# Kernel optimization log

Measured on AMD Instinct MI355X. Metric: run time of the kernel, lower is better.

The kernel has to match this reference:

```python
import jax, jax.numpy as jnp
import numpy as np

K = 3
STRIDE = 1
PAD = 1
C_IN = 128
C_OUT = 256

def setup_inputs() -> dict:
    key = jax.random.key(0)
    kx, kw, kb = jax.random.split(key, 3)
    x = jax.random.normal(kx, (32, C_IN, 56, 56), dtype=jnp.float32)
    # torch init: uniform(-1/K, 1/K) for kernels, uniform(-1/sqrt(Cout), 1/sqrt(Cout)) for bias
    kernels = jax.random.uniform(kw, (C_OUT, C_IN, K, K), dtype=jnp.float32,
                                 minval=-1.0 / K, maxval=1.0 / K)
    b = jax.random.uniform(kb, (C_OUT,), dtype=jnp.float32,
                           minval=-1.0 / C_OUT ** 0.5, maxval=1.0 / C_OUT ** 0.5)
    return {"x": x, "kernels": kernels, "b": b}

def reference(x, kernels, b):
    # Same math as the im2col broadcast-matmul + channel-sum: a standard 2D conv
    # with zero padding, expressed as one contracted GEMM via conv_general_dilated.
    out = jax.lax.conv_general_dilated(
        x, kernels,
        window_strides=(STRIDE, STRIDE),
        padding=((PAD, PAD), (PAD, PAD)),
        dimension_numbers=("NCHW", "OIHW", "NCHW"),
    )
    return out + b.reshape(1, C_OUT, 1, 1)
```

## Files before the change

kernel.cpp:

```cpp
#include <hip/hip_runtime.h>
#include <hip/hip_bf16.h>

#define NB   32
#define CIN  128
#define COUT 256
#define HH   56
#define WW   56

typedef __attribute__((ext_vector_type(8))) short short8;
typedef __attribute__((ext_vector_type(4))) float f32x4;

__device__ __forceinline__ unsigned short f2bf(float f) {
    unsigned int u = __builtin_bit_cast(unsigned int, f);
    u = u + 0x7fffu + ((u >> 16) & 1u);
    return (unsigned short)(u >> 16);
}

__global__ __launch_bounds__(256) void wpose_kernel(const float* __restrict__ w,
                                                    unsigned short* __restrict__ wt2) {
    int q = blockIdx.x * 256 + threadIdx.x;
    if (q >= 36 * 16 * 64 * 8) return;
    int j = q & 7;
    int l = (q >> 3) & 63;
    int f = (q >> 9) & 15;
    int s = q >> 13;
    int g = l >> 4, r = l & 15;
    int t = s >> 2, cc = s & 3;
    int o = f * 16 + r;
    int c = cc * 32 + g * 8 + j;
    wt2[q] = f2bf(w[((size_t)o * CIN + c) * 9 + t]);
}

__global__ __launch_bounds__(1024, 4) void conv_mfma_kernel(
        const float* __restrict__ x,
        const unsigned short* __restrict__ wt2,
        const float* __restrict__ bias,
        float* __restrict__ out) {
    __shared__ unsigned short ldsB[6 * 16 * 58 * 8];

    const int tid  = threadIdx.x;
    const int h0   = blockIdx.x * 4, n = blockIdx.y;
    const int wid  = tid >> 6, lane = tid & 63;
    const int wm   = wid >> 1, wn = wid & 1;
    const int g    = lane >> 4, r = lane & 15;

    for (int i = tid; i < 6 * 16 * 58; i += 1024) {
        uint4 z = {0u, 0u, 0u, 0u};
        *(uint4*)&ldsB[(size_t)i * 8] = z;
    }
    __syncthreads();

    {
        const float* xn = x + (size_t)n * CIN * HH * WW;
        for (int i = tid; i < 6 * 64 * 14; i += 1024) {
            int w4  = i % 14;
            int t1  = i / 14;
            int cp  = t1 & 63;
            int row = t1 >> 6;
            int hs  = h0 + row - 1;
            if ((unsigned)hs < HH) {
                const float* src = xn + ((size_t)(2 * cp) * HH + hs) * WW + 4 * w4;
                float4 va = *(const float4*)src;
                float4 vb = *(const float4*)(src + HH * WW);
                int gc = cp >> 2, e = cp & 3;
                #pragma unroll
                for (int j = 0; j < 4; ++j) {
                    int wpos = 4 * w4 + j + 1;
                    unsigned int pk = (unsigned int)f2bf(((const float*)&va)[j])
                                    | ((unsigned int)f2bf(((const float*)&vb)[j]) << 16);
                    ((unsigned int*)ldsB)[((row * 16 + gc) * 58 + wpos) * 4 + e] = pk;
                }
            }
        }
    }
    __syncthreads();

    int lo[7];
    #pragma unroll
    for (int ni = 0; ni < 7; ++ni) {
        int c  = ni * 16 + r;
        int hr = (c >= 56) ? 1 : 0;
        lo[ni] = hr * (16 * 58) + (c - hr * 56);
    }

    f32x4 acc[2][7];
    #pragma unroll
    for (int mi = 0; mi < 2; ++mi)
        #pragma unroll
        for (int ni = 0; ni < 7; ++ni)
            #pragma unroll
            for (int v = 0; v < 4; ++v) acc[mi][ni][v] = 0.f;

    const short8* abase = (const short8*)wt2 + (size_t)(wm * 2) * 64 + lane;

    #pragma unroll
    for (int t = 0; t < 9; ++t) {
        const int kh = t / 3, kw = t % 3;
        #pragma unroll
        for (int cc = 0; cc < 4; ++cc) {
            const int s  = t * 4 + cc;
            const int gc = cc * 4 + g;
            const int bb = (((wn * 2 + kh) * 16 + gc) * 58 + kw);

            short8 a[2];
            #pragma unroll
            for (int mi = 0; mi < 2; ++mi)
                a[mi] = abase[(size_t)s * 1024 + mi * 64];

            short8 b[7];
            #pragma unroll
            for (int ni = 0; ni < 7; ++ni)
                b[ni] = *(const short8*)&ldsB[(size_t)(bb + lo[ni]) * 8];

            #pragma unroll
            for (int mi = 0; mi < 2; ++mi)
                #pragma unroll
                for (int ni = 0; ni < 7; ++ni)
                    acc[mi][ni] = __builtin_amdgcn_mfma_f32_16x16x32_bf16(
                        a[mi], b[ni], acc[mi][ni], 0, 0, 0);
        }
    }

    #pragma unroll
    for (int mi = 0; mi < 2; ++mi) {
        const int o0 = wm * 32 + mi * 16 + 4 * g;
        const float4 bv = *(const float4*)&bias[o0];
        #pragma unroll
        for (int ni = 0; ni < 7; ++ni) {
            const int c  = ni * 16 + r;
            const int hr = (c >= 56) ? 1 : 0;
            const int h  = h0 + wn * 2 + hr;
            const int w  = c - hr * 56;
            #pragma unroll
            for (int v = 0; v < 4; ++v) {
                out[((size_t)(n * COUT + o0 + v) * HH + h) * WW + w] =
                    acc[mi][ni][v] + ((const float*)&bv)[v];
            }
        }
    }
}

extern "C" void kernel_launch(void* const* d_in, const int* in_sizes, int n_in,
                              void* d_out, int out_size, void* d_ws, size_t ws_size,
                              hipStream_t stream) {
    const float* x  = (const float*)d_in[0];
    const float* wk = (const float*)d_in[1];
    const float* b  = (const float*)d_in[2];
    float* out = (float*)d_out;

    unsigned short* wt2 = (unsigned short*)d_ws;

    wpose_kernel<<<(36 * 16 * 64 * 8 + 255) / 256, 256, 0, stream>>>(wk, wt2);
    dim3 gc(14, NB);
    conv_mfma_kernel<<<gc, 1024, 0, stream>>>(x, wt2, b, out);
    (void)ws_size; (void)in_sizes; (void)n_in; (void)out_size;
}
```

Baseline: 77.41 us.

## Re-tile conv waves to 128 output channels by 32 pixels and simplify staging

Changes the per-wave tile from 32 output channels by 112 pixels to 128 channels by 32 pixels, spread over 2x8 waves. Each wave now loads 8 A fragments from global weights and only 2 B fragments from LDS per step, cutting LDS reads but raising global weight traffic per wave. The last wave column pads to 256 pixels and masks stores, so some MFMA work is wasted. Input staging switches from float4 loads to scalar per-element loads with one lane per channel pair, which may lower global load efficiency.

```diff
diff --git a/kernel.cpp b/kernel.cpp
--- a/kernel.cpp
+++ b/kernel.cpp
@@ -41,7 +41,7 @@
     const int tid  = threadIdx.x;
     const int h0   = blockIdx.x * 4, n = blockIdx.y;
     const int wid  = tid >> 6, lane = tid & 63;
-    const int wm   = wid >> 1, wn = wid & 1;
+    const int wm   = wid >> 3, wn = wid & 7;
     const int g    = lane >> 4, r = lane & 15;
 
     for (int i = tid; i < 6 * 16 * 58; i += 1024) {
@@ -52,89 +52,85 @@
 
     {
         const float* xn = x + (size_t)n * CIN * HH * WW;
-        for (int i = tid; i < 6 * 64 * 14; i += 1024) {
-            int w4  = i % 14;
-            int t1  = i / 14;
-            int cp  = t1 & 63;
-            int row = t1 >> 6;
+        const int cp = tid & 63, e = cp & 3, gcq = cp >> 2;
+        const float* pc = xn + (size_t)(2 * cp) * (HH * WW);
+        for (int rw = tid >> 6; rw < 6 * 56; rw += 16) {
+            int row = rw / 56, w = rw - row * 56;
             int hs  = h0 + row - 1;
             if ((unsigned)hs < HH) {
-                const float* src = xn + ((size_t)(2 * cp) * HH + hs) * WW + 4 * w4;
-                float4 va = *(const float4*)src;
-                float4 vb = *(const float4*)(src + HH * WW);
-                int gc = cp >> 2, e = cp & 3;
-                #pragma unroll
-                for (int j = 0; j < 4; ++j) {
-                    int wpos = 4 * w4 + j + 1;
-                    unsigned int pk = (unsigned int)f2bf(((const float*)&va)[j])
-                                    | ((unsigned int)f2bf(((const float*)&vb)[j]) << 16);
-                    ((unsigned int*)ldsB)[((row * 16 + gc) * 58 + wpos) * 4 + e] = pk;
-                }
+                const float* p = pc + hs * WW + w;
+                unsigned int pk = (unsigned int)f2bf(p[0])
+                                | ((unsigned int)f2bf(p[HH * WW]) << 16);
+                ((unsigned int*)ldsB)[((row * 16 + gcq) * 58 + (w + 1)) * 4 + e] = pk;
             }
         }
     }
     __syncthreads();
 
-    int lo[7];
+    int hrv[2], wv[2], base2[2];
+    bool ok[2];
     #pragma unroll
-    for (int ni = 0; ni < 7; ++ni) {
-        int c  = ni * 16 + r;
-        int hr = (c >= 56) ? 1 : 0;
-        lo[ni] = hr * (16 * 58) + (c - hr * 56);
+    for (int ni = 0; ni < 2; ++ni) {
+        int c = wn * 32 + ni * 16 + r;
+        ok[ni] = (c < 224);
+        int hr, w;
+        if (ok[ni]) { hr = c / 56; w = c - hr * 56; }
+        else        { hr = 3;      w = c & 31; }
+        hrv[ni] = hr; wv[ni] = w;
+        base2[ni] = hr * 928 + g * 58 + w;
     }
 
-    f32x4 acc[2][7];
+    f32x4 acc[8][2];
     #pragma unroll
-    for (int mi = 0; mi < 2; ++mi)
+    for (int mi = 0; mi < 8; ++mi)
         #pragma unroll
-        for (int ni = 0; ni < 7; ++ni)
+        for (int ni = 0; ni < 2; ++ni)
             #pragma unroll
             for (int v = 0; v < 4; ++v) acc[mi][ni][v] = 0.f;
 
-    const short8* abase = (const short8*)wt2 + (size_t)(wm * 2) * 64 + lane;
+    const short8* abase = (const short8*)wt2 + (size_t)(wm * 8) * 64 + lane;
 
     #pragma unroll
     for (int t = 0; t < 9; ++t) {
         const int kh = t / 3, kw = t % 3;
         #pragma unroll
         for (int cc = 0; cc < 4; ++cc) {
-            const int s  = t * 4 + cc;
-            const int gc = cc * 4 + g;
-            const int bb = (((wn * 2 + kh) * 16 + gc) * 58 + kw);
+            const int s = t * 4 + cc;
 
-            short8 a[2];
+            short8 a[8];
             #pragma unroll
-            for (int mi = 0; mi < 2; ++mi)
+            for (int mi = 0; mi < 8; ++mi)
                 a[mi] = abase[(size_t)s * 1024 + mi * 64];
 
-            short8 b[7];
+            const int koff = kh * 928 + cc * 232 + kw;
+            short8 b[2];
             #pragma unroll
-            for (int ni = 0; ni < 7; ++ni)
-                b[ni] = *(const short8*)&ldsB[(size_t)(bb + lo[ni]) * 8];
+            for (int ni = 0; ni < 2; ++ni)
+                b[ni] = *(const short8*)&ldsB[(size_t)(base2[ni] + koff) * 8];
 
             #pragma unroll
-            for (int mi = 0; mi < 2; ++mi)
+            for (int mi = 0; mi < 8; ++mi)
                 #pragma unroll
-                for (int ni = 0; ni < 7; ++ni)
+                for (int ni = 0; ni < 2; ++ni)
                     acc[mi][ni] = __builtin_amdgcn_mfma_f32_16x16x32_bf16(
                         a[mi], b[ni], acc[mi][ni], 0, 0, 0);
         }
     }
 
     #pragma unroll
-    for (int mi = 0; mi < 2; ++mi) {
-        const int o0 = wm * 32 + mi * 16 + 4 * g;
+    for (int mi = 0; mi < 8; ++mi) {
+        const int o0 = wm * 128 + mi * 16 + 4 * g;
         const float4 bv = *(const float4*)&bias[o0];
         #pragma unroll
-        for (int ni = 0; ni < 7; ++ni) {
-            const int c  = ni * 16 + r;
-            const int hr = (c >= 56) ? 1 : 0;
-            const int h  = h0 + wn * 2 + hr;
-            const int w  = c - hr * 56;
-            #pragma unroll
-            for (int v = 0; v < 4; ++v) {
-                out[((size_t)(n * COUT + o0 + v) * HH + h) * WW + w] =
-                    acc[mi][ni][v] + ((const float*)&bv)[v];
+        for (int ni = 0; ni < 2; ++ni) {
+            if (ok[ni]) {
+                const int h = h0 + hrv[ni];
+                const int w = wv[ni];
+                #pragma unroll
+                for (int v = 0; v < 4; ++v) {
+                    out[((size_t)(n * COUT + o0 + v) * HH + h) * WW + w] =
+                        acc[mi][ni][v] + ((const float*)&bv)[v];
+                }
             }
         }
     }
```

New measurement: 225.4 us. +191.2%, slower.

## Stage weights in LDS via async global-to-LDS loads with double buffering

Applied to the files above, without the earlier changes.

The block size drops from 1024 to 512 threads and each wave computes 64 output channels instead of 32, doubling accumulator tiles per wave so each B fragment read from LDS feeds more MFMAs. Weight fragments are now double-buffered in LDS through global_load_lds, with a barrier after every K-step, instead of being loaded straight from global memory. The input staging loop is rewritten so each lane handles one channel pair with scalar loads. The aim is to reuse each weight load across waves and to overlap weight fetches with compute. The costs are higher register pressure, 36 barriers per block, and less coalesced scalar input loads.

```diff
diff --git a/kernel.cpp b/kernel.cpp
--- a/kernel.cpp
+++ b/kernel.cpp
@@ -16,6 +16,13 @@
     return (unsigned short)(u >> 16);
 }
 
+__device__ __forceinline__ void glds16(const unsigned short* g, unsigned short* l) {
+    __builtin_amdgcn_global_load_lds(
+        (const __attribute__((address_space(1))) unsigned int*)g,
+        (__attribute__((address_space(3))) unsigned int*)l,
+        16, 0, 0);
+}
+
 __global__ __launch_bounds__(256) void wpose_kernel(const float* __restrict__ w,
                                                     unsigned short* __restrict__ wt2) {
     int q = blockIdx.x * 256 + threadIdx.x;
@@ -31,12 +38,13 @@
     wt2[q] = f2bf(w[((size_t)o * CIN + c) * 9 + t]);
 }
 
-__global__ __launch_bounds__(1024, 4) void conv_mfma_kernel(
+__global__ __launch_bounds__(512, 2) void conv_mfma_kernel(
         const float* __restrict__ x,
         const unsigned short* __restrict__ wt2,
         const float* __restrict__ bias,
         float* __restrict__ out) {
     __shared__ unsigned short ldsB[6 * 16 * 58 * 8];
+    __shared__ unsigned short ldsA[2][16 * 64 * 8];
 
     const int tid  = threadIdx.x;
     const int h0   = blockIdx.x * 4, n = blockIdx.y;
@@ -44,7 +52,7 @@
     const int wm   = wid >> 1, wn = wid & 1;
     const int g    = lane >> 4, r = lane & 15;
 
-    for (int i = tid; i < 6 * 16 * 58; i += 1024) {
+    for (int i = tid; i < 6 * 16 * 58; i += 512) {
         uint4 z = {0u, 0u, 0u, 0u};
         *(uint4*)&ldsB[(size_t)i * 8] = z;
     }
@@ -52,27 +60,30 @@
 
     {
         const float* xn = x + (size_t)n * CIN * HH * WW;
-        for (int i = tid; i < 6 * 64 * 14; i += 1024) {
-            int w4  = i % 14;
-            int t1  = i / 14;
-            int cp  = t1 & 63;
-            int row = t1 >> 6;
+        const int cp = lane, e = cp & 3, gcq = cp >> 2;
+        const float* pc = xn + (size_t)(2 * cp) * (HH * WW);
+        for (int rw = wid; rw < 6 * 56; rw += 8) {
+            int row = rw / 56, w = rw - row * 56;
             int hs  = h0 + row - 1;
             if ((unsigned)hs < HH) {
-                const float* src = xn + ((size_t)(2 * cp) * HH + hs) * WW + 4 * w4;
-                float4 va = *(const float4*)src;
-                float4 vb = *(const float4*)(src + HH * WW);
-                int gc = cp >> 2, e = cp & 3;
-                #pragma unroll
-                for (int j = 0; j < 4; ++j) {
-                    int wpos = 4 * w4 + j + 1;
-                    unsigned int pk = (unsigned int)f2bf(((const float*)&va)[j])
-                                    | ((unsigned int)f2bf(((const float*)&vb)[j]) << 16);
-                    ((unsigned int*)ldsB)[((row * 16 + gc) * 58 + wpos) * 4 + e] = pk;
-                }
+                const float* p = pc + hs * WW + w;
+                unsigned int pk = (unsigned int)f2bf(p[0])
+                                | ((unsigned int)f2bf(p[HH * WW]) << 16);
+                ((unsigned int*)ldsB)[((row * 16 + gcq) * 58 + (w + 1)) * 4 + e] = pk;
             }
         }
     }
+
+    #define STAGE_A(buf, s)                                                     \
+        {                                                                       \
+            const unsigned short* asrc = wt2 + (size_t)(s) * (16 * 64 * 8);     \
+            glds16(asrc + (size_t)(wid * 64 + lane) * 8,                        \
+                   &ldsA[buf][(size_t)(wid * 64) * 8]);                         \
+            glds16(asrc + (size_t)(512 + wid * 64 + lane) * 8,                  \
+                   &ldsA[buf][(size_t)(512 + wid * 64) * 8]);                   \
+        }
+
+    STAGE_A(0, 0);
     __syncthreads();
 
     int lo[7];
@@ -83,47 +94,48 @@
         lo[ni] = hr * (16 * 58) + (c - hr * 56);
     }
 
-    f32x4 acc[2][7];
+    f32x4 acc[4][7];
     #pragma unroll
-    for (int mi = 0; mi < 2; ++mi)
+    for (int mi = 0; mi < 4; ++mi)
         #pragma unroll
         for (int ni = 0; ni < 7; ++ni)
             #pragma unroll
             for (int v = 0; v < 4; ++v) acc[mi][ni][v] = 0.f;
 
-    const short8* abase = (const short8*)wt2 + (size_t)(wm * 2) * 64 + lane;
+    int cur = 0;
+    #pragma unroll 1
+    for (int s = 0; s < 36; ++s) {
+        if (s < 35) STAGE_A(cur ^ 1, s + 1);
 
-    #pragma unroll
-    for (int t = 0; t < 9; ++t) {
-        const int kh = t / 3, kw = t % 3;
+        const int t  = s >> 2, cc = s & 3;
+        const int kh = t / 3, kw = t - 3 * (t / 3);
+        const int gc = cc * 4 + g;
+        const int bb = (((wn * 2 + kh) * 16 + gc) * 58 + kw);
+
+        short8 a[4];
         #pragma unroll
-        for (int cc = 0; cc < 4; ++cc) {
-            const int s  = t * 4 + cc;
-            const int gc = cc * 4 + g;
-            const int bb = (((wn * 2 + kh) * 16 + gc) * 58 + kw);
+        for (int mi = 0; mi < 4; ++mi)
+            a[mi] = *(const short8*)&ldsA[cur][(size_t)(((wm * 4 + mi) * 64 + lane)) * 8];
 
-            short8 a[2];
-            #pragma unroll
-            for (int mi = 0; mi < 2; ++mi)
-                a[mi] = abase[(size_t)s * 1024 + mi * 64];
+        short8 b[7];
+        #pragma unroll
+        for (int ni = 0; ni < 7; ++ni)
+            b[ni] = *(const short8*)&ldsB[(size_t)(bb + lo[ni]) * 8];
 
-            short8 b[7];
+        #pragma unroll
+        for (int mi = 0; mi < 4; ++mi)
             #pragma unroll
             for (int ni = 0; ni < 7; ++ni)
-                b[ni] = *(const short8*)&ldsB[(size_t)(bb + lo[ni]) * 8];
+                acc[mi][ni] = __builtin_amdgcn_mfma_f32_16x16x32_bf16(
+                    a[mi], b[ni], acc[mi][ni], 0, 0, 0);
 
-            #pragma unroll
-            for (int mi = 0; mi < 2; ++mi)
-                #pragma unroll
-                for (int ni = 0; ni < 7; ++ni)
-                    acc[mi][ni] = __builtin_amdgcn_mfma_f32_16x16x32_bf16(
-                        a[mi], b[ni], acc[mi][ni], 0, 0, 0);
-        }
+        __syncthreads();
+        cur ^= 1;
     }
 
     #pragma unroll
-    for (int mi = 0; mi < 2; ++mi) {
-        const int o0 = wm * 32 + mi * 16 + 4 * g;
+    for (int mi = 0; mi < 4; ++mi) {
+        const int o0 = wm * 64 + mi * 16 + 4 * g;
         const float4 bv = *(const float4*)&bias[o0];
         #pragma unroll
         for (int ni = 0; ni < 7; ++ni) {
@@ -152,6 +164,6 @@
 
     wpose_kernel<<<(36 * 16 * 64 * 8 + 255) / 256, 256, 0, stream>>>(wk, wt2);
     dim3 gc(14, NB);
-    conv_mfma_kernel<<<gc, 1024, 0, stream>>>(x, wt2, b, out);
+    conv_mfma_kernel<<<gc, 512, 0, stream>>>(x, wt2, b, out);
     (void)ws_size; (void)in_sizes; (void)n_in; (void)out_size;
 }
```

Result: slower. 119.7 us (+54.6%).
